# Kernel optimization log

Hardware: AMD Instinct MI355X
Metric: run time of the kernel (lower is better)

Reference implementation:

```python
import jax, jax.numpy as jnp
import numpy as np

D_MODEL = 1024
D_STATE = 8          # max(8, 16 // 2)
D_CONV = 4
D_INNER = int(1.5 * D_MODEL)   # expand = max(1.5, 2*0.75)
DT_RANK = (D_MODEL + 15) // 16 # 64
D_FF = 2 * D_MODEL
B, L = 2, 2048


def layer_norm(x, g, b, eps=1e-5):
    mu = jnp.mean(x, -1, keepdims=True)
    var = jnp.var(x, -1, keepdims=True)
    return (x - mu) * jax.lax.rsqrt(var + eps) * g + b


def setup_inputs() -> dict:
    key = jax.random.key(0)
    ks = jax.random.split(key, 12)
    def n(k, shape, scale=0.02):
        return jax.random.normal(k, shape, dtype=jnp.float32) * scale
    return {
        'x': jax.random.normal(ks[0], (B, L, D_MODEL), dtype=jnp.float32),
        'ln1_g': jnp.ones((D_MODEL,), jnp.float32),
        'ln1_b': jnp.zeros((D_MODEL,), jnp.float32),
        'ln2_g': jnp.ones((D_MODEL,), jnp.float32),
        'ln2_b': jnp.zeros((D_MODEL,), jnp.float32),
        'in_proj_w': n(ks[1], (2 * D_INNER, D_MODEL)),
        'conv_w': n(ks[2], (D_INNER, 1, D_CONV), 0.1),
        'conv_b': jnp.zeros((D_INNER,), jnp.float32),
        'x_proj_w': n(ks[3], (DT_RANK + 2 * D_STATE, D_INNER)),
        'dt_proj_w': n(ks[4], (D_INNER, DT_RANK), 0.1),
        'dt_proj_b': n(ks[5], (D_INNER,), 0.1),
        'A_log': jnp.log(jnp.broadcast_to(jnp.arange(1, D_STATE + 1, dtype=jnp.float32), (D_INNER, D_STATE))),
        'D': jnp.ones((D_INNER,), jnp.float32),
        'out_proj_w': n(ks[6], (D_MODEL, D_INNER)),
        'ffn_w1': n(ks[7], (D_FF, D_MODEL)),
        'ffn_b1': jnp.zeros((D_FF,), jnp.float32),
        'ffn_w2': n(ks[8], (D_MODEL, D_FF)),
        'ffn_b2': jnp.zeros((D_MODEL,), jnp.float32),
    }


def mamba(x, in_proj_w, conv_w, conv_b, x_proj_w, dt_proj_w, dt_proj_b, A_log, Dp, out_proj_w):
    # in_proj -> (x, z)
    xz = x @ in_proj_w.T                       # (B, L, 2*d_inner)
    xi, z = jnp.split(xz, 2, axis=-1)
    # depthwise causal conv over seq, kernel 4
    xc = jnp.transpose(xi, (0, 2, 1))          # (B, d_inner, L)
    xc = jax.lax.conv_general_dilated(
        xc, conv_w, window_strides=(1,), padding=[(D_CONV - 1, 0)],
        dimension_numbers=('NCH', 'OIH', 'NCH'), feature_group_count=D_INNER)
    xc = xc + conv_b[None, :, None]
    u = jax.nn.silu(jnp.transpose(xc, (0, 2, 1)))  # (B, L, d_inner)
    # x_proj -> dt, B, C
    x_dbl = u @ x_proj_w.T
    dt = x_dbl[..., :DT_RANK]
    Bm = x_dbl[..., DT_RANK:DT_RANK + D_STATE]
    Cm = x_dbl[..., DT_RANK + D_STATE:]
    delta = jax.nn.softplus(dt @ dt_proj_w.T + dt_proj_b)  # (B, L, d_inner)
    A = -jnp.exp(A_log)                                    # (d_inner, d_state)
    dA = jnp.exp(jnp.einsum('bld,dn->bldn', delta, A))     # (B, L, d_inner, d_state)
    dBu = jnp.einsum('bld,bln,bld->bldn', delta, Bm, u)
    # selective scan over time
    def step(h, inputs):
        dA_t, dBu_t, C_t = inputs
        h = dA_t * h + dBu_t                   # (B, d_inner, d_state)
        y = jnp.einsum('bdn,bn->bd', h, C_t)
        return h, y
    h0 = jnp.zeros((x.shape[0], D_INNER, D_STATE), x.dtype)
    _, ys = jax.lax.scan(step, h0, (jnp.moveaxis(dA, 1, 0), jnp.moveaxis(dBu, 1, 0), jnp.moveaxis(Cm, 1, 0)))
    y = jnp.moveaxis(ys, 0, 1) + u * Dp        # skip connection D*u
    y = y * jax.nn.silu(z)                     # gate
    return y @ out_proj_w.T


def reference(x, ln1_g, ln1_b, ln2_g, ln2_b, in_proj_w, conv_w, conv_b, x_proj_w,
              dt_proj_w, dt_proj_b, A_log, D, out_proj_w, ffn_w1, ffn_b1, ffn_w2, ffn_b2):
    residual = x
    xp = layer_norm(x, ln1_g, ln1_b)
    x = mamba(xp, in_proj_w, conv_w, conv_b, x_proj_w, dt_proj_w, dt_proj_b, A_log, D, out_proj_w) + residual
    xn = layer_norm(x, ln2_g, ln2_b)
    h = jax.nn.gelu(xn @ ffn_w1.T + ffn_b1, approximate=False)  # dropout is identity in eval
    return x + (h @ ffn_w2.T + ffn_b2)
```

## Files before the change

### kernel.cpp

```cpp
#include <hip/hip_runtime.h>
#include <math.h>

#define D_MODEL 1024
#define D_STATE 8
#define D_CONV  4
#define D_INNER 1536
#define DT_RANK 64
#define D_FF    2048
#define BATCH   2
#define SEQ     2048
#define NROWS   (BATCH*SEQ)
#define NC      32
#define LC      (SEQ/NC)
#define XPAD    128

typedef short bf16x8 __attribute__((ext_vector_type(8)));
typedef unsigned short u16x8 __attribute__((ext_vector_type(8)));
typedef float f32x4  __attribute__((ext_vector_type(4)));

__device__ inline unsigned short f2bf(float x) {
    union { float f; unsigned u; } v; v.f = x;
    unsigned r = v.u + 0x7fffu + ((v.u >> 16) & 1u);
    return (unsigned short)(r >> 16);
}
__device__ inline float bf2f(unsigned short h) {
    union { unsigned u; float f; } v; v.u = ((unsigned)h) << 16;
    return v.f;
}
__device__ inline float softplus_f(float x) {
    return (x > 20.0f) ? x : log1pf(__expf(x));
}
__device__ inline float gelu_f(float x) {
    return 0.5f * x * (1.0f + erff(x * 0.70710678118654752f));
}
__device__ inline float silu_f(float x) {
    return x / (1.0f + __expf(-x));
}
__device__ inline void gload16(const unsigned short* g, unsigned short* l) {
    typedef unsigned int u32;
    __builtin_amdgcn_global_load_lds(
        (const __attribute__((address_space(1))) u32*)g,
        (__attribute__((address_space(3))) u32*)l, 16, 0, 0);
}

#define PHASE_SYNC_PRE()  do { __builtin_amdgcn_s_barrier(); __builtin_amdgcn_sched_barrier(0); \
                               asm volatile("s_waitcnt lgkmcnt(0)" ::: "memory"); \
                               __builtin_amdgcn_sched_barrier(0); } while (0)
#define PHASE_SYNC_POST() do { __builtin_amdgcn_s_barrier(); __builtin_amdgcn_sched_barrier(0); } while (0)

__global__ __launch_bounds__(256) void wconv(const float* __restrict__ s0, unsigned short* __restrict__ d0,
                                             const float* __restrict__ s1, unsigned short* __restrict__ d1,
                                             const float* __restrict__ s2, unsigned short* __restrict__ d2,
                                             const float* __restrict__ s3, unsigned short* __restrict__ d3,
                                             const float* __restrict__ s4, unsigned short* __restrict__ d4) {
    int b = blockIdx.x;
    const float* s; unsigned short* d; int base;
    if      (b < 1536) { s = s0; d = d0; base = b * 2048; }
    else if (b < 1584) { s = s1; d = d1; base = (b - 1536) * 2048; }
    else if (b < 2352) { s = s2; d = d2; base = (b - 1584) * 2048; }
    else if (b < 3376) { s = s3; d = d3; base = (b - 2352) * 2048; }
    else               { s = s4; d = d4; base = (b - 3376) * 2048; }
    int i = base + threadIdx.x * 8;
    float4 v0 = *(const float4*)(s + i);
    float4 v1 = *(const float4*)(s + i + 4);
    ushort4 a, c;
    a.x = f2bf(v0.x); a.y = f2bf(v0.y); a.z = f2bf(v0.z); a.w = f2bf(v0.w);
    c.x = f2bf(v1.x); c.y = f2bf(v1.y); c.z = f2bf(v1.z); c.w = f2bf(v1.w);
    *(ushort4*)(d + i)     = a;
    *(ushort4*)(d + i + 4) = c;
}

__global__ __launch_bounds__(256) void xproj_pad(const float* __restrict__ src, unsigned short* __restrict__ dst) {
    int row = blockIdx.x;
    for (int c = threadIdx.x; c < D_INNER; c += 256)
        dst[row * D_INNER + c] = (row < 80) ? f2bf(src[row * D_INNER + c]) : (unsigned short)0;
}

__global__ __launch_bounds__(256) void ln_kernel(const float* __restrict__ x,
                                                 const float* __restrict__ g,
                                                 const float* __restrict__ b,
                                                 unsigned short* __restrict__ out) {
    __shared__ float sbuf[4];
    int row = blockIdx.x;
    int t = threadIdx.x;
    const float4* xr = (const float4*)(x + (size_t)row * D_MODEL);
    float4 v = xr[t];
    float s = v.x + v.y + v.z + v.w;
    for (int o = 32; o; o >>= 1) s += __shfl_down(s, o, 64);
    if ((t & 63) == 0) sbuf[t >> 6] = s;
    __syncthreads();
    float mu = (sbuf[0] + sbuf[1] + sbuf[2] + sbuf[3]) * (1.0f / D_MODEL);
    __syncthreads();
    float d0 = v.x - mu, d1 = v.y - mu, d2 = v.z - mu, d3 = v.w - mu;
    float q = d0*d0 + d1*d1 + d2*d2 + d3*d3;
    for (int o = 32; o; o >>= 1) q += __shfl_down(q, o, 64);
    if ((t & 63) == 0) sbuf[t >> 6] = q;
    __syncthreads();
    float var = (sbuf[0] + sbuf[1] + sbuf[2] + sbuf[3]) * (1.0f / D_MODEL);
    float rs = rsqrtf(var + 1e-5f);
    float4 gv = ((const float4*)g)[t];
    float4 bv = ((const float4*)b)[t];
    ushort4 st;
    st.x = f2bf(d0 * rs * gv.x + bv.x);
    st.y = f2bf(d1 * rs * gv.y + bv.y);
    st.z = f2bf(d2 * rs * gv.z + bv.z);
    st.w = f2bf(d3 * rs * gv.w + bv.w);
    ((ushort4*)(out + (size_t)row * D_MODEL))[t] = st;
}

#define EPI_F32        0
#define EPI_F32_BF16   1
#define EPI_SOFTPLUS   2
#define EPI_RESID      3
#define EPI_GELU_BF16  4
#define EPI_BIAS_RESID 5
#define EPI_BF16       6

template<int WN, int EPI, int SPLITK>
__global__ __launch_bounds__(512, 2) void gemm8p(
    const unsigned short* __restrict__ A, int lda,
    const unsigned short* __restrict__ Bm, int ldb, int K,
    float* __restrict__ Cf, unsigned short* __restrict__ Cb, int ldc,
    const float* __restrict__ bias,
    const float* __restrict__ resid, int ldr) {
    constexpr int WM = 8 / WN;
    constexpr int BN = WN * 64;
    constexpr int RW = 256 / WM;
    constexpr int CW = 64;
    constexpr int MI = RW / 16;
    constexpr int NI = CW / 16;
    constexpr int MIH = MI / 2, NIH = NI / 2;
    constexpr int ABYTES = 256 * 128;
    constexpr int BBYTES = BN * 128;
    constexpr int BOFF = 2 * ABYTES;
    __shared__ unsigned short lds[(2 * ABYTES + 2 * BBYTES) / 2];

    const int t = threadIdx.x, l = t & 63, w = t >> 6;
    const int wr = w / WN, wc = w % WN;

    const int nx = gridDim.x;
    const int nwg = nx * gridDim.y;
    int bid = blockIdx.y * nx + blockIdx.x;
    int q = nwg >> 3;
    int swz = (bid & 7) * q + (bid >> 3);
    const int m0 = (swz / nx) * 256, n0 = (swz % nx) * BN;
    const int kbase = (SPLITK > 1) ? blockIdx.z * K : 0;

    const int sr = l >> 3;
    const int sj = ((l & 7) * 16) ^ ((l >> 3) << 4);
    const int row_l = w * 8;
    const int row_c = (w >> 2) * 64 + (w & 3) * 8;

    auto STG = [&](int bufbyte, int rowbase, const unsigned short* G, int ldg, int gbase, int kt) {
        unsigned short* dst = (unsigned short*)((char*)lds + bufbyte + rowbase * 128);
        const unsigned short* src = G + (size_t)(gbase + rowbase + sr) * ldg + kbase + kt * 64 + (sj >> 1);
        gload16(src, dst);
    };
    auto S_Ah0 = [&](int b, int kt) {
        if (WN == 4) { STG(b * ABYTES, row_l, A, lda, m0, kt);       STG(b * ABYTES, 128 + row_l, A, lda, m0, kt); }
        else         { STG(b * ABYTES, row_c, A, lda, m0, kt);       STG(b * ABYTES, 128 + row_c, A, lda, m0, kt); }
    };
    auto S_Ah1 = [&](int b, int kt) {
        if (WN == 4) { STG(b * ABYTES, 64 + row_l, A, lda, m0, kt);  STG(b * ABYTES, 192 + row_l, A, lda, m0, kt); }
        else         { STG(b * ABYTES, 32 + row_c, A, lda, m0, kt);  STG(b * ABYTES, 160 + row_c, A, lda, m0, kt); }
    };
    auto S_Bc0 = [&](int b, int kt) {
        if (WN == 4) { STG(BOFF + b * BBYTES, row_c, Bm, ldb, n0, kt); STG(BOFF + b * BBYTES, 128 + row_c, Bm, ldb, n0, kt); }
        else         { STG(BOFF + b * BBYTES, row_c, Bm, ldb, n0, kt); }
    };
    auto S_Bc1 = [&](int b, int kt) {
        if (WN == 4) { STG(BOFF + b * BBYTES, 32 + row_c, Bm, ldb, n0, kt); STG(BOFF + b * BBYTES, 160 + row_c, Bm, ldb, n0, kt); }
        else         { STG(BOFF + b * BBYTES, 32 + row_c, Bm, ldb, n0, kt); }
    };

    auto LD = [&](int bytebase, int row, int kb) -> bf16x8 {
        int o = bytebase + row * 128 + (kb ^ ((row & 7) << 4));
        return *(const bf16x8*)((const char*)lds + o);
    };

    f32x4 acc[MI][NI] = {};
    bf16x8 af[MIH][2], b0v[NIH][2], b1v[NIH][2];

    auto LDA_set = [&](int buf, int qr, auto& dst) {
        #pragma unroll
        for (int mi = 0; mi < MIH; mi++)
            #pragma unroll
            for (int ks = 0; ks < 2; ks++)
                dst[mi][ks] = LD(buf * ABYTES, wr * RW + qr * (RW / 2) + mi * 16 + (l & 15),
                                 ks * 64 + (l >> 4) * 16);
    };
    auto LDB_set = [&](int buf, int qc, auto& dst) {
        #pragma unroll
        for (int ni2 = 0; ni2 < NIH; ni2++)
            #pragma unroll
            for (int ks = 0; ks < 2; ks++)
                dst[ni2][ks] = LD(BOFF + buf * BBYTES, wc * CW + qc * 32 + ni2 * 16 + (l & 15),
                                  ks * 64 + (l >> 4) * 16);
    };
    auto MFMA_Q = [&](int qr, int qc, auto& a_, auto& b_) {
        __builtin_amdgcn_s_setprio(1);
        #pragma unroll
        for (int mi = 0; mi < MIH; mi++)
            #pragma unroll
            for (int ni2 = 0; ni2 < NIH; ni2++)
                #pragma unroll
                for (int ks = 0; ks < 2; ks++)
                    acc[qr * MIH + mi][qc * NIH + ni2] =
                        __builtin_amdgcn_mfma_f32_16x16x32_bf16(a_[mi][ks], b_[ni2][ks],
                                                                acc[qr * MIH + mi][qc * NIH + ni2], 0, 0, 0);
        __builtin_amdgcn_s_setprio(0);
    };
    auto VMW = [&](bool last) {
        if (last)            asm volatile("s_waitcnt vmcnt(0)" ::: "memory");
        else if (WN == 4)    asm volatile("s_waitcnt vmcnt(6)" ::: "memory");
        else                 asm volatile("s_waitcnt vmcnt(5)" ::: "memory");
        __builtin_amdgcn_sched_barrier(0);
    };

    const int ni_ = K >> 7;

    S_Ah0(0, 0); S_Ah1(0, 0); S_Bc0(0, 0); S_Bc1(0, 0);
    S_Ah0(1, 1); S_Ah1(1, 1); S_Bc0(1, 1); S_Bc1(1, 1);
    if (WN == 4) asm volatile("s_waitcnt vmcnt(8)" ::: "memory");
    else         asm volatile("s_waitcnt vmcnt(6)" ::: "memory");
    __builtin_amdgcn_s_barrier();
    __builtin_amdgcn_sched_barrier(0);

    for (int i = 0; i < ni_; i++) {
        const bool last = (i == ni_ - 1);
        const int t2 = 2 * i + 2, t3 = 2 * i + 3;
        LDA_set(0, 0, af); LDB_set(0, 0, b0v);
        if (i) S_Bc0(1, 2 * i + 1);
        PHASE_SYNC_PRE(); MFMA_Q(0, 0, af, b0v); PHASE_SYNC_POST();
        LDB_set(0, 1, b1v);
        if (!last) S_Ah0(0, t2);
        PHASE_SYNC_PRE(); MFMA_Q(0, 1, af, b1v); PHASE_SYNC_POST();
        LDA_set(0, 1, af);
        PHASE_SYNC_PRE(); MFMA_Q(1, 1, af, b1v); PHASE_SYNC_POST();
        LDB_set(0, 0, b0v);
        if (!last) { S_Ah1(0, t2); S_Bc1(0, t2); }
        VMW(last);
        PHASE_SYNC_PRE(); MFMA_Q(1, 0, af, b0v); PHASE_SYNC_POST();
        LDA_set(1, 0, af); LDB_set(1, 0, b0v);
        if (!last) S_Bc0(0, t2);
        PHASE_SYNC_PRE(); MFMA_Q(0, 0, af, b0v); PHASE_SYNC_POST();
        LDB_set(1, 1, b1v);
        if (!last) S_Ah0(1, t3);
        PHASE_SYNC_PRE(); MFMA_Q(0, 1, af, b1v); PHASE_SYNC_POST();
        LDA_set(1, 1, af);
        PHASE_SYNC_PRE(); MFMA_Q(1, 1, af, b1v); PHASE_SYNC_POST();
        LDB_set(1, 0, b0v);
        if (!last) { S_Ah1(1, t3); S_Bc1(1, t3); }
        VMW(last);
        PHASE_SYNC_PRE(); MFMA_Q(1, 0, af, b0v); PHASE_SYNC_POST();
    }

    float* Cfp = Cf;
    if (SPLITK > 1) Cfp += (size_t)blockIdx.z * NROWS * ldc;
    #pragma unroll
    for (int ni2 = 0; ni2 < NI; ni2++) {
        int col = n0 + wc * CW + ni2 * 16 + (l & 15);
        float bv = 0.0f;
        if (EPI == EPI_SOFTPLUS || EPI == EPI_GELU_BF16 || EPI == EPI_BIAS_RESID) bv = bias[col];
        #pragma unroll
        for (int mi = 0; mi < MI; mi++) {
            #pragma unroll
            for (int j = 0; j < 4; j++) {
                int row = m0 + wr * RW + mi * 16 + (l >> 4) * 4 + j;
                float v = acc[mi][ni2][j];
                if (EPI == EPI_SOFTPLUS)        v = softplus_f(v + bv);
                else if (EPI == EPI_GELU_BF16)  v = gelu_f(v + bv);
                else if (EPI == EPI_RESID)      v = v + resid[(size_t)row * ldr + col];
                else if (EPI == EPI_BIAS_RESID) v = v + bv + resid[(size_t)row * ldr + col];
                if (EPI == EPI_GELU_BF16 || EPI == EPI_BF16) {
                    Cb[(size_t)row * ldc + col] = f2bf(v);
                } else {
                    Cfp[(size_t)row * ldc + col] = v;
                    if (EPI == EPI_F32_BF16) Cb[(size_t)row * ldc + col] = f2bf(v);
                }
            }
        }
    }
}

template<int WITH_BIAS>
__global__ __launch_bounds__(256) void sk2_reduce(const float* __restrict__ p,
                                                  const float* __restrict__ bias,
                                                  const float* __restrict__ resid,
                                                  float* __restrict__ o) {
    int i = (blockIdx.x * 256 + threadIdx.x) * 4;
    const size_t seg = (size_t)NROWS * D_MODEL;
    float4 a = *(const float4*)(p + i);
    float4 b = *(const float4*)(p + i + seg);
    float4 r = *(const float4*)(resid + i);
    float4 o4;
    if (WITH_BIAS) {
        float4 bb = *(const float4*)(bias + (i & (D_MODEL - 1)));
        o4.x = a.x + b.x + r.x + bb.x;
        o4.y = a.y + b.y + r.y + bb.y;
        o4.z = a.z + b.z + r.z + bb.z;
        o4.w = a.w + b.w + r.w + bb.w;
    } else {
        o4.x = a.x + b.x + r.x;
        o4.y = a.y + b.y + r.y;
        o4.z = a.z + b.z + r.z;
        o4.w = a.w + b.w + r.w;
    }
    *(float4*)(o + i) = o4;
}

template<int EPI, int SPLITK>
__global__ __launch_bounds__(256) void gemm_mfma(
    const unsigned short* __restrict__ A, int lda,
    const unsigned short* __restrict__ B, int ldb, int K,
    float* __restrict__ Cf, unsigned short* __restrict__ Cb, int ldc,
    const float* __restrict__ bias,
    const float* __restrict__ resid, int ldr) {
    __shared__ unsigned short As[3][128 * 32];
    __shared__ unsigned short Bs[3][128 * 32];
    int t = threadIdx.x, l = t & 63, w = t >> 6;
    int nx = gridDim.x;
    int nwg = nx * gridDim.y;
    int bid = blockIdx.y * nx + blockIdx.x;
    int q = nwg >> 3;
    int swz = (bid & 7) * q + (bid >> 3);
    int m0 = (swz / nx) * 128, n0 = (swz % nx) * 128;
    int kbase = (SPLITK > 1) ? blockIdx.z * K : 0;
    int c0 = 2 * w, c1 = 2 * w + 1;
    int srow = l >> 2, scol = (l & 3) * 8;
    const unsigned short* Ag0 = A + (size_t)(m0 + 16 * c0 + srow) * lda + kbase + scol;
    const unsigned short* Ag1 = A + (size_t)(m0 + 16 * c1 + srow) * lda + kbase + scol;
    const unsigned short* Bg0 = B + (size_t)(n0 + 16 * c0 + srow) * ldb + kbase + scol;
    const unsigned short* Bg1 = B + (size_t)(n0 + 16 * c1 + srow) * ldb + kbase + scol;
    int wr = w >> 1, wc = w & 1;
    int aoff = (wr * 64 + (l & 15)) * 32 + (l >> 4) * 8;
    int boff = (wc * 64 + (l & 15)) * 32 + (l >> 4) * 8;

    f32x4 acc[4][4] = {};
    int nt = K >> 5;

    gload16(Ag0, &As[0][c0 * 512]);
    gload16(Ag1, &As[0][c1 * 512]);
    gload16(Bg0, &Bs[0][c0 * 512]);
    gload16(Bg1, &Bs[0][c1 * 512]);
    if (nt > 1) {
        gload16(Ag0 + 32, &As[1][c0 * 512]);
        gload16(Ag1 + 32, &As[1][c1 * 512]);
        gload16(Bg0 + 32, &Bs[1][c0 * 512]);
        gload16(Bg1 + 32, &Bs[1][c1 * 512]);
    }

    int cur = 0;
    for (int ti = 0; ti < nt; ti++) {
        int pf = ti + 2;
        if (pf < nt) {
            int nb = cur - 1; if (nb < 0) nb += 3;
            int k0 = pf << 5;
            gload16(Ag0 + k0, &As[nb][c0 * 512]);
            gload16(Ag1 + k0, &As[nb][c1 * 512]);
            gload16(Bg0 + k0, &Bs[nb][c0 * 512]);
            gload16(Bg1 + k0, &Bs[nb][c1 * 512]);
        }
        int rem = nt - 1 - ti;
        if (rem >= 2)      asm volatile("s_waitcnt vmcnt(8)" ::: "memory");
        else if (rem == 1) asm volatile("s_waitcnt vmcnt(4)" ::: "memory");
        else               asm volatile("s_waitcnt vmcnt(0)" ::: "memory");
        __builtin_amdgcn_s_barrier();

        const unsigned short* Ab = &As[cur][0];
        const unsigned short* Bb = &Bs[cur][0];
        bf16x8 af[4], bfv[4];
        #pragma unroll
        for (int i = 0; i < 4; i++) af[i] = *(const bf16x8*)(Ab + aoff + i * 512);
        #pragma unroll
        for (int i = 0; i < 4; i++) bfv[i] = *(const bf16x8*)(Bb + boff + i * 512);
        __builtin_amdgcn_s_setprio(1);
        #pragma unroll
        for (int mi = 0; mi < 4; mi++)
            #pragma unroll
            for (int ni = 0; ni < 4; ni++)
                acc[mi][ni] = __builtin_amdgcn_mfma_f32_16x16x32_bf16(af[mi], bfv[ni], acc[mi][ni], 0, 0, 0);
        __builtin_amdgcn_s_setprio(0);
        __builtin_amdgcn_s_barrier();
        cur++; if (cur == 3) cur = 0;
    }

    if (SPLITK > 1) Cf += (size_t)blockIdx.z * NROWS * ldc;
    int colb = n0 + wc * 64 + (l & 15);
    int rowb = m0 + wr * 64 + (l >> 4) * 4;
    #pragma unroll
    for (int ni = 0; ni < 4; ni++) {
        int col = colb + ni * 16;
        float bv = 0.0f;
        if (EPI == EPI_SOFTPLUS || EPI == EPI_GELU_BF16 || EPI == EPI_BIAS_RESID) bv = bias[col];
        #pragma unroll
        for (int mi = 0; mi < 4; mi++) {
            #pragma unroll
            for (int j = 0; j < 4; j++) {
                int row = rowb + mi * 16 + j;
                float v = acc[mi][ni][j];
                if (EPI == EPI_SOFTPLUS)        v = softplus_f(v + bv);
                else if (EPI == EPI_GELU_BF16)  v = gelu_f(v + bv);
                else if (EPI == EPI_RESID)      v = v + resid[(size_t)row * ldr + col];
                else if (EPI == EPI_BIAS_RESID) v = v + bv + resid[(size_t)row * ldr + col];
                if (EPI == EPI_GELU_BF16 || EPI == EPI_BF16) {
                    Cb[(size_t)row * ldc + col] = f2bf(v);
                } else {
                    Cf[(size_t)row * ldc + col] = v;
                    if (EPI == EPI_F32_BF16) Cb[(size_t)row * ldc + col] = f2bf(v);
                }
            }
        }
    }
}

__global__ __launch_bounds__(256) void xdbl_reduce(const float* __restrict__ part,
                                                   float* __restrict__ xdbl,
                                                   unsigned short* __restrict__ xdbl_bf) {
    int i = blockIdx.x * 256 + threadIdx.x;
    const size_t seg = (size_t)NROWS * XPAD;
    float s = part[i] + part[i + seg] + part[i + 2 * seg] + part[i + 3 * seg];
    xdbl[i] = s;
    xdbl_bf[i] = f2bf(s);
}

__global__ __launch_bounds__(256) void conv_silu(const unsigned short* __restrict__ xz,
                                                 const float* __restrict__ w,
                                                 const float* __restrict__ cb,
                                                 unsigned short* __restrict__ u) {
    int idx = (blockIdx.x * 256 + threadIdx.x) * 8;
    int d = idx % D_INNER;
    int bl = idx / D_INNER;
    int l = bl & (SEQ - 1);
    float acc[8];
    float4 wv[8];
    #pragma unroll
    for (int j = 0; j < 8; j++) wv[j] = *(const float4*)(w + (d + j) * 4);
    float4 cb0 = *(const float4*)(cb + d);
    float4 cb1 = *(const float4*)(cb + d + 4);
    acc[0] = cb0.x; acc[1] = cb0.y; acc[2] = cb0.z; acc[3] = cb0.w;
    acc[4] = cb1.x; acc[5] = cb1.y; acc[6] = cb1.z; acc[7] = cb1.w;
    #pragma unroll
    for (int k = 0; k < 4; k++) {
        int lp = l - 3 + k;
        if (lp >= 0) {
            u16x8 s = *(const u16x8*)(xz + (size_t)(bl - 3 + k) * (2 * D_INNER) + d);
            #pragma unroll
            for (int j = 0; j < 8; j++) {
                float wk = (k == 0) ? wv[j].x : (k == 1) ? wv[j].y : (k == 2) ? wv[j].z : wv[j].w;
                acc[j] += bf2f((unsigned short)s[j]) * wk;
            }
        }
    }
    u16x8 o;
    #pragma unroll
    for (int j = 0; j < 8; j++) o[j] = f2bf(silu_f(acc[j]));
    *(u16x8*)(u + idx) = o;
}

__global__ __launch_bounds__(256) void scan_passA(const float* __restrict__ delta,
                                                  const unsigned short* __restrict__ u,
                                                  const float* __restrict__ xdbl,
                                                  const float* __restrict__ A_log,
                                                  float* __restrict__ P,
                                                  float* __restrict__ S) {
    int d = blockIdx.x * 256 + threadIdx.x;
    int c = blockIdx.y, b = blockIdx.z;
    __shared__ float bc[LC][16];
    int base_row = b * SEQ + c * LC;
    for (int e = threadIdx.x; e < LC * 16; e += 256) {
        int lrr = e >> 4, col = e & 15;
        bc[lrr][col] = xdbl[(size_t)(base_row + lrr) * XPAD + DT_RANK + col];
    }
    __syncthreads();
    float Ad[8];
    #pragma unroll
    for (int n = 0; n < 8; n++) Ad[n] = -__expf(A_log[d * 8 + n]);
    float prod[8], hs[8];
    #pragma unroll
    for (int n = 0; n < 8; n++) { prod[n] = 1.0f; hs[n] = 0.0f; }
    for (int lrr = 0; lrr < LC; lrr++) {
        int row = base_row + lrr;
        float dl = delta[(size_t)row * D_INNER + d];
        float uu = bf2f(u[(size_t)row * D_INNER + d]);
        float du = dl * uu;
        #pragma unroll
        for (int n = 0; n < 8; n++) {
            float dA = __expf(dl * Ad[n]);
            prod[n] *= dA;
            hs[n] = dA * hs[n] + du * bc[lrr][n];
        }
    }
    size_t o = ((size_t)((size_t)b * NC + c) * D_INNER + d) * 8;
    #pragma unroll
    for (int n = 0; n < 8; n++) { P[o + n] = prod[n]; S[o + n] = hs[n]; }
}

__global__ __launch_bounds__(256) void scan_passB(const float* __restrict__ P,
                                                  const float* __restrict__ S,
                                                  float* __restrict__ hstart) {
    int tid = blockIdx.x * 256 + threadIdx.x;
    int b = tid / (D_INNER * 8);
    int rem = tid % (D_INNER * 8);
    float h = 0.0f;
    for (int c = 0; c < NC; c++) {
        size_t o = (size_t)(b * NC + c) * (D_INNER * 8) + rem;
        hstart[o] = h;
        h = P[o] * h + S[o];
    }
}

__global__ __launch_bounds__(256) void scan_passC(const float* __restrict__ delta,
                                                  const unsigned short* __restrict__ u,
                                                  const float* __restrict__ xdbl,
                                                  const float* __restrict__ A_log,
                                                  const float* __restrict__ hstart,
                                                  const unsigned short* __restrict__ xz,
                                                  const float* __restrict__ Dp,
                                                  unsigned short* __restrict__ ygate) {
    int d = blockIdx.x * 256 + threadIdx.x;
    int c = blockIdx.y, b = blockIdx.z;
    __shared__ float bc[LC][16];
    int base_row = b * SEQ + c * LC;
    for (int e = threadIdx.x; e < LC * 16; e += 256) {
        int lrr = e >> 4, col = e & 15;
        bc[lrr][col] = xdbl[(size_t)(base_row + lrr) * XPAD + DT_RANK + col];
    }
    __syncthreads();
    float Ad[8];
    #pragma unroll
    for (int n = 0; n < 8; n++) Ad[n] = -__expf(A_log[d * 8 + n]);
    float h[8];
    size_t ho = ((size_t)((size_t)b * NC + c) * D_INNER + d) * 8;
    #pragma unroll
    for (int n = 0; n < 8; n++) h[n] = hstart[ho + n];
    float Dd = Dp[d];
    for (int lrr = 0; lrr < LC; lrr++) {
        int row = base_row + lrr;
        float dl = delta[(size_t)row * D_INNER + d];
        float uu = bf2f(u[(size_t)row * D_INNER + d]);
        float du = dl * uu;
        float y = 0.0f;
        #pragma unroll
        for (int n = 0; n < 8; n++) {
            float dA = __expf(dl * Ad[n]);
            h[n] = dA * h[n] + du * bc[lrr][n];
            y += h[n] * bc[lrr][8 + n];
        }
        y += uu * Dd;
        float z = bf2f(xz[(size_t)row * (2 * D_INNER) + D_INNER + d]);
        ygate[(size_t)row * D_INNER + d] = f2bf(y * silu_f(z));
    }
}

extern "C" void kernel_launch(void* const* d_in, const int* in_sizes, int n_in,
                              void* d_out, int out_size, void* d_ws, size_t ws_size,
                              hipStream_t stream) {
    const float* x         = (const float*)d_in[0];
    const float* ln1_g     = (const float*)d_in[1];
    const float* ln1_b     = (const float*)d_in[2];
    const float* ln2_g     = (const float*)d_in[3];
    const float* ln2_b     = (const float*)d_in[4];
    const float* in_proj_w = (const float*)d_in[5];
    const float* conv_w    = (const float*)d_in[6];
    const float* conv_b    = (const float*)d_in[7];
    const float* x_proj_w  = (const float*)d_in[8];
    const float* dt_proj_w = (const float*)d_in[9];
    const float* dt_proj_b = (const float*)d_in[10];
    const float* A_log     = (const float*)d_in[11];
    const float* Dp        = (const float*)d_in[12];
    const float* out_proj_w= (const float*)d_in[13];
    const float* ffn_w1    = (const float*)d_in[14];
    const float* ffn_b1    = (const float*)d_in[15];
    const float* ffn_w2    = (const float*)d_in[16];
    const float* ffn_b2    = (const float*)d_in[17];
    float* out = (float*)d_out;

    float* xdbl  = (float*)d_ws;
    float* delta = xdbl + (size_t)NROWS * XPAD;
    float* P     = delta + (size_t)NROWS * D_INNER;
    float* S     = P + (size_t)BATCH * NC * D_INNER * 8;
    float* hst   = S + (size_t)BATCH * NC * D_INNER * 8;
    float* x2    = hst + (size_t)BATCH * NC * D_INNER * 8;
    float* part  = x2;
    float* psum  = delta;
    unsigned short* xz_bf   = (unsigned short*)(x2 + (size_t)NROWS * D_MODEL);
    unsigned short* xp_bf   = xz_bf + (size_t)NROWS * 2 * D_INNER;
    unsigned short* u_bf    = xp_bf + (size_t)NROWS * D_MODEL;
    unsigned short* xdbl_bf = u_bf + (size_t)NROWS * D_INNER;
    unsigned short* yg_bf   = xdbl_bf + (size_t)NROWS * XPAD;
    unsigned short* w_in    = yg_bf + (size_t)NROWS * D_INNER;
    unsigned short* w_xp    = w_in + (size_t)2 * D_INNER * D_MODEL;
    unsigned short* w_dt    = w_xp + (size_t)XPAD * D_INNER;
    unsigned short* w_out   = w_dt + (size_t)D_INNER * DT_RANK;
    unsigned short* w_f1    = w_out + (size_t)D_MODEL * D_INNER;
    unsigned short* w_f2    = w_f1 + (size_t)D_FF * D_MODEL;
    unsigned short* hff_bf  = xz_bf;

    wconv<<<4400, 256, 0, stream>>>(in_proj_w, w_in, dt_proj_w, w_dt, out_proj_w, w_out,
                                    ffn_w1, w_f1, ffn_w2, w_f2);
    xproj_pad<<<XPAD, 256, 0, stream>>>(x_proj_w, w_xp);
    ln_kernel<<<NROWS, 256, 0, stream>>>(x, ln1_g, ln1_b, xp_bf);
    gemm8p<4, EPI_BF16, 1><<<dim3(3072 / 256, NROWS / 256), 512, 0, stream>>>(
        xp_bf, D_MODEL, w_in, D_MODEL, D_MODEL, nullptr, xz_bf, 2 * D_INNER, nullptr, nullptr, 0);
    conv_silu<<<(NROWS * D_INNER) / (256 * 8), 256, 0, stream>>>(xz_bf, conv_w, conv_b, u_bf);
    gemm_mfma<EPI_F32, 4><<<dim3(1, NROWS / 128, 4), 256, 0, stream>>>(
        u_bf, D_INNER, w_xp, D_INNER, D_INNER / 4, part, nullptr, XPAD, nullptr, nullptr, 0);
    xdbl_reduce<<<(NROWS * XPAD) / 256, 256, 0, stream>>>(part, xdbl, xdbl_bf);
    gemm_mfma<EPI_SOFTPLUS, 1><<<dim3(D_INNER / 128, NROWS / 128), 256, 0, stream>>>(
        xdbl_bf, XPAD, w_dt, DT_RANK, DT_RANK, delta, nullptr, D_INNER, dt_proj_b, nullptr, 0);
    scan_passA<<<dim3(D_INNER / 256, NC, BATCH), 256, 0, stream>>>(delta, u_bf, xdbl, A_log, P, S);
    scan_passB<<<(BATCH * D_INNER * 8) / 256, 256, 0, stream>>>(P, S, hst);
    scan_passC<<<dim3(D_INNER / 256, NC, BATCH), 256, 0, stream>>>(delta, u_bf, xdbl, A_log, hst, xz_bf, Dp, yg_bf);
    gemm8p<2, EPI_F32, 2><<<dim3(D_MODEL / 128, NROWS / 256, 2), 512, 0, stream>>>(
        yg_bf, D_INNER, w_out, D_INNER, D_INNER / 2, psum, nullptr, D_MODEL, nullptr, nullptr, 0);
    sk2_reduce<0><<<(NROWS * D_MODEL) / 1024, 256, 0, stream>>>(psum, nullptr, x, x2);
    ln_kernel<<<NROWS, 256, 0, stream>>>(x2, ln2_g, ln2_b, xp_bf);
    gemm8p<2, EPI_GELU_BF16, 1><<<dim3(D_FF / 128, NROWS / 256), 512, 0, stream>>>(
        xp_bf, D_MODEL, w_f1, D_MODEL, D_MODEL, nullptr, hff_bf, D_FF, ffn_b1, nullptr, 0);
    gemm8p<2, EPI_F32, 2><<<dim3(D_MODEL / 128, NROWS / 256, 2), 512, 0, stream>>>(
        hff_bf, D_FF, w_f2, D_FF, D_FF / 2, psum, nullptr, D_MODEL, nullptr, nullptr, 0);
    sk2_reduce<1><<<(NROWS * D_MODEL) / 1024, 256, 0, stream>>>(psum, ffn_b2, x2, out);
}
```

Before: 290.4 us.

## Fuse prep kernels, fuse split-K reduce with LayerNorm, store delta as bf16

Merges the weight conversion, x_proj padding and first LayerNorm into one prep kernel, and fuses the out_proj split-K reduction with the second LayerNorm. Stores the softplus delta output in bf16 instead of fp32, which halves the scan passes' delta traffic at some cost in precision. Removes the sched_barrier calls around the gemm8p phase syncs and the vmcnt waits, which gives the compiler more freedom to schedule but may break the hand-tuned ordering. Also reorganizes the workspace so psum no longer aliases delta.

Result: faster. 281.1 us (-3.2%).

```diff
diff --git a/kernel.cpp b/kernel.cpp
--- a/kernel.cpp
+++ b/kernel.cpp
@@ -43,37 +43,66 @@
         (__attribute__((address_space(3))) u32*)l, 16, 0, 0);
 }
 
-#define PHASE_SYNC_PRE()  do { __builtin_amdgcn_s_barrier(); __builtin_amdgcn_sched_barrier(0); \
-                               asm volatile("s_waitcnt lgkmcnt(0)" ::: "memory"); \
-                               __builtin_amdgcn_sched_barrier(0); } while (0)
-#define PHASE_SYNC_POST() do { __builtin_amdgcn_s_barrier(); __builtin_amdgcn_sched_barrier(0); } while (0)
-
-__global__ __launch_bounds__(256) void wconv(const float* __restrict__ s0, unsigned short* __restrict__ d0,
-                                             const float* __restrict__ s1, unsigned short* __restrict__ d1,
-                                             const float* __restrict__ s2, unsigned short* __restrict__ d2,
-                                             const float* __restrict__ s3, unsigned short* __restrict__ d3,
-                                             const float* __restrict__ s4, unsigned short* __restrict__ d4) {
+#define PHASE_SYNC_PRE()  do { __builtin_amdgcn_s_barrier(); \
+                               asm volatile("s_waitcnt lgkmcnt(0)" ::: "memory"); } while (0)
+#define PHASE_SYNC_POST() do { __builtin_amdgcn_s_barrier(); } while (0)
+
+__global__ __launch_bounds__(256) void prep_kernel(
+    const float* __restrict__ s0, unsigned short* __restrict__ d0,
+    const float* __restrict__ s1, unsigned short* __restrict__ d1,
+    const float* __restrict__ s2, unsigned short* __restrict__ d2,
+    const float* __restrict__ s3, unsigned short* __restrict__ d3,
+    const float* __restrict__ s4, unsigned short* __restrict__ d4,
+    const float* __restrict__ xpw, unsigned short* __restrict__ xpd,
+    const float* __restrict__ x, const float* __restrict__ g1,
+    const float* __restrict__ b1, unsigned short* __restrict__ xout) {
     int b = blockIdx.x;
-    const float* s; unsigned short* d; int base;
-    if      (b < 1536) { s = s0; d = d0; base = b * 2048; }
-    else if (b < 1584) { s = s1; d = d1; base = (b - 1536) * 2048; }
-    else if (b < 2352) { s = s2; d = d2; base = (b - 1584) * 2048; }
-    else if (b < 3376) { s = s3; d = d3; base = (b - 2352) * 2048; }
-    else               { s = s4; d = d4; base = (b - 3376) * 2048; }
-    int i = base + threadIdx.x * 8;
-    float4 v0 = *(const float4*)(s + i);
-    float4 v1 = *(const float4*)(s + i + 4);
-    ushort4 a, c;
-    a.x = f2bf(v0.x); a.y = f2bf(v0.y); a.z = f2bf(v0.z); a.w = f2bf(v0.w);
-    c.x = f2bf(v1.x); c.y = f2bf(v1.y); c.z = f2bf(v1.z); c.w = f2bf(v1.w);
-    *(ushort4*)(d + i)     = a;
-    *(ushort4*)(d + i + 4) = c;
-}
-
-__global__ __launch_bounds__(256) void xproj_pad(const float* __restrict__ src, unsigned short* __restrict__ dst) {
-    int row = blockIdx.x;
-    for (int c = threadIdx.x; c < D_INNER; c += 256)
-        dst[row * D_INNER + c] = (row < 80) ? f2bf(src[row * D_INNER + c]) : (unsigned short)0;
+    if (b < 4400) {
+        const float* s; unsigned short* d; int base;
+        if      (b < 1536) { s = s0; d = d0; base = b * 2048; }
+        else if (b < 1584) { s = s1; d = d1; base = (b - 1536) * 2048; }
+        else if (b < 2352) { s = s2; d = d2; base = (b - 1584) * 2048; }
+        else if (b < 3376) { s = s3; d = d3; base = (b - 2352) * 2048; }
+        else               { s = s4; d = d4; base = (b - 3376) * 2048; }
+        int i = base + threadIdx.x * 8;
+        float4 v0 = *(const float4*)(s + i);
+        float4 v1 = *(const float4*)(s + i + 4);
+        ushort4 a, c;
+        a.x = f2bf(v0.x); a.y = f2bf(v0.y); a.z = f2bf(v0.z); a.w = f2bf(v0.w);
+        c.x = f2bf(v1.x); c.y = f2bf(v1.y); c.z = f2bf(v1.z); c.w = f2bf(v1.w);
+        *(ushort4*)(d + i)     = a;
+        *(ushort4*)(d + i + 4) = c;
+    } else if (b < 4528) {
+        int row = b - 4400;
+        for (int c = threadIdx.x; c < D_INNER; c += 256)
+            xpd[row * D_INNER + c] = (row < 80) ? f2bf(xpw[row * D_INNER + c]) : (unsigned short)0;
+    } else {
+        __shared__ float sbuf[4];
+        int row = b - 4528;
+        int t = threadIdx.x;
+        float4 v = ((const float4*)(x + (size_t)row * D_MODEL))[t];
+        float s = v.x + v.y + v.z + v.w;
+        for (int o = 32; o; o >>= 1) s += __shfl_down(s, o, 64);
+        if ((t & 63) == 0) sbuf[t >> 6] = s;
+        __syncthreads();
+        float mu = (sbuf[0] + sbuf[1] + sbuf[2] + sbuf[3]) * (1.0f / D_MODEL);
+        __syncthreads();
+        float e0 = v.x - mu, e1 = v.y - mu, e2 = v.z - mu, e3 = v.w - mu;
+        float q = e0*e0 + e1*e1 + e2*e2 + e3*e3;
+        for (int o = 32; o; o >>= 1) q += __shfl_down(q, o, 64);
+        if ((t & 63) == 0) sbuf[t >> 6] = q;
+        __syncthreads();
+        float var = (sbuf[0] + sbuf[1] + sbuf[2] + sbuf[3]) * (1.0f / D_MODEL);
+        float rs = rsqrtf(var + 1e-5f);
+        float4 gv = ((const float4*)g1)[t];
+        float4 bv = ((const float4*)b1)[t];
+        ushort4 st;
+        st.x = f2bf(e0 * rs * gv.x + bv.x);
+        st.y = f2bf(e1 * rs * gv.y + bv.y);
+        st.z = f2bf(e2 * rs * gv.z + bv.z);
+        st.w = f2bf(e3 * rs * gv.w + bv.w);
+        ((ushort4*)(xout + (size_t)row * D_MODEL))[t] = st;
+    }
 }
 
 __global__ __launch_bounds__(256) void ln_kernel(const float* __restrict__ x,
@@ -83,8 +112,7 @@
     __shared__ float sbuf[4];
     int row = blockIdx.x;
     int t = threadIdx.x;
-    const float4* xr = (const float4*)(x + (size_t)row * D_MODEL);
-    float4 v = xr[t];
+    float4 v = ((const float4*)(x + (size_t)row * D_MODEL))[t];
     float s = v.x + v.y + v.z + v.w;
     for (int o = 32; o; o >>= 1) s += __shfl_down(s, o, 64);
     if ((t & 63) == 0) sbuf[t >> 6] = s;
@@ -115,6 +143,7 @@
 #define EPI_GELU_BF16  4
 #define EPI_BIAS_RESID 5
 #define EPI_BF16       6
+#define EPI_SOFTPLUS_BF16 7
 
 template<int WN, int EPI, int SPLITK>
 __global__ __launch_bounds__(512, 2) void gemm8p(
@@ -214,7 +243,6 @@
         if (last)            asm volatile("s_waitcnt vmcnt(0)" ::: "memory");
         else if (WN == 4)    asm volatile("s_waitcnt vmcnt(6)" ::: "memory");
         else                 asm volatile("s_waitcnt vmcnt(5)" ::: "memory");
-        __builtin_amdgcn_sched_barrier(0);
     };
 
     const int ni_ = K >> 7;
@@ -224,7 +252,6 @@
     if (WN == 4) asm volatile("s_waitcnt vmcnt(8)" ::: "memory");
     else         asm volatile("s_waitcnt vmcnt(6)" ::: "memory");
     __builtin_amdgcn_s_barrier();
-    __builtin_amdgcn_sched_barrier(0);
 
     for (int i = 0; i < ni_; i++) {
         const bool last = (i == ni_ - 1);
@@ -283,7 +310,49 @@
     }
 }
 
-template<int WITH_BIAS>
+__global__ __launch_bounds__(256) void sk2_ln(const float* __restrict__ p,
+                                              const float* __restrict__ resid,
+                                              const float* __restrict__ g,
+                                              const float* __restrict__ b,
+                                              float* __restrict__ x2,
+                                              unsigned short* __restrict__ xn) {
+    __shared__ float sbuf[4];
+    int row = blockIdx.x;
+    int t = threadIdx.x;
+    const size_t seg = (size_t)NROWS * D_MODEL;
+    size_t base = (size_t)row * D_MODEL + t * 4;
+    float4 a = *(const float4*)(p + base);
+    float4 bb = *(const float4*)(p + base + seg);
+    float4 r = *(const float4*)(resid + base);
+    float4 v;
+    v.x = a.x + bb.x + r.x;
+    v.y = a.y + bb.y + r.y;
+    v.z = a.z + bb.z + r.z;
+    v.w = a.w + bb.w + r.w;
+    *(float4*)(x2 + base) = v;
+    float s = v.x + v.y + v.z + v.w;
+    for (int o = 32; o; o >>= 1) s += __shfl_down(s, o, 64);
+    if ((t & 63) == 0) sbuf[t >> 6] = s;
+    __syncthreads();
+    float mu = (sbuf[0] + sbuf[1] + sbuf[2] + sbuf[3]) * (1.0f / D_MODEL);
+    __syncthreads();
+    float d0 = v.x - mu, d1 = v.y - mu, d2 = v.z - mu, d3 = v.w - mu;
+    float qq = d0*d0 + d1*d1 + d2*d2 + d3*d3;
+    for (int o = 32; o; o >>= 1) qq += __shfl_down(qq, o, 64);
+    if ((t & 63) == 0) sbuf[t >> 6] = qq;
+    __syncthreads();
+    float var = (sbuf[0] + sbuf[1] + sbuf[2] + sbuf[3]) * (1.0f / D_MODEL);
+    float rs = rsqrtf(var + 1e-5f);
+    float4 gv = ((const float4*)g)[t];
+    float4 bv = ((const float4*)b)[t];
+    ushort4 st;
+    st.x = f2bf(d0 * rs * gv.x + bv.x);
+    st.y = f2bf(d1 * rs * gv.y + bv.y);
+    st.z = f2bf(d2 * rs * gv.z + bv.z);
+    st.w = f2bf(d3 * rs * gv.w + bv.w);
+    ((ushort4*)(xn + (size_t)row * D_MODEL))[t] = st;
+}
+
 __global__ __launch_bounds__(256) void sk2_reduce(const float* __restrict__ p,
                                                   const float* __restrict__ bias,
                                                   const float* __restrict__ resid,
@@ -293,19 +362,12 @@
     float4 a = *(const float4*)(p + i);
     float4 b = *(const float4*)(p + i + seg);
     float4 r = *(const float4*)(resid + i);
+    float4 bb = *(const float4*)(bias + (i & (D_MODEL - 1)));
     float4 o4;
-    if (WITH_BIAS) {
-        float4 bb = *(const float4*)(bias + (i & (D_MODEL - 1)));
-        o4.x = a.x + b.x + r.x + bb.x;
-        o4.y = a.y + b.y + r.y + bb.y;
-        o4.z = a.z + b.z + r.z + bb.z;
-        o4.w = a.w + b.w + r.w + bb.w;
-    } else {
-        o4.x = a.x + b.x + r.x;
-        o4.y = a.y + b.y + r.y;
-        o4.z = a.z + b.z + r.z;
-        o4.w = a.w + b.w + r.w;
-    }
+    o4.x = a.x + b.x + r.x + bb.x;
+    o4.y = a.y + b.y + r.y + bb.y;
+    o4.z = a.z + b.z + r.z + bb.z;
+    o4.w = a.w + b.w + r.w + bb.w;
     *(float4*)(o + i) = o4;
 }
 
@@ -392,18 +454,18 @@
     for (int ni = 0; ni < 4; ni++) {
         int col = colb + ni * 16;
         float bv = 0.0f;
-        if (EPI == EPI_SOFTPLUS || EPI == EPI_GELU_BF16 || EPI == EPI_BIAS_RESID) bv = bias[col];
+        if (EPI == EPI_SOFTPLUS || EPI == EPI_GELU_BF16 || EPI == EPI_BIAS_RESID || EPI == EPI_SOFTPLUS_BF16) bv = bias[col];
         #pragma unroll
         for (int mi = 0; mi < 4; mi++) {
             #pragma unroll
             for (int j = 0; j < 4; j++) {
                 int row = rowb + mi * 16 + j;
                 float v = acc[mi][ni][j];
-                if (EPI == EPI_SOFTPLUS)        v = softplus_f(v + bv);
+                if (EPI == EPI_SOFTPLUS || EPI == EPI_SOFTPLUS_BF16) v = softplus_f(v + bv);
                 else if (EPI == EPI_GELU_BF16)  v = gelu_f(v + bv);
                 else if (EPI == EPI_RESID)      v = v + resid[(size_t)row * ldr + col];
                 else if (EPI == EPI_BIAS_RESID) v = v + bv + resid[(size_t)row * ldr + col];
-                if (EPI == EPI_GELU_BF16 || EPI == EPI_BF16) {
+                if (EPI == EPI_GELU_BF16 || EPI == EPI_BF16 || EPI == EPI_SOFTPLUS_BF16) {
                     Cb[(size_t)row * ldc + col] = f2bf(v);
                 } else {
                     Cf[(size_t)row * ldc + col] = v;
@@ -458,7 +520,7 @@
     *(u16x8*)(u + idx) = o;
 }
 
-__global__ __launch_bounds__(256) void scan_passA(const float* __restrict__ delta,
+__global__ __launch_bounds__(256) void scan_passA(const unsigned short* __restrict__ delta,
                                                   const unsigned short* __restrict__ u,
                                                   const float* __restrict__ xdbl,
                                                   const float* __restrict__ A_log,
@@ -481,7 +543,7 @@
     for (int n = 0; n < 8; n++) { prod[n] = 1.0f; hs[n] = 0.0f; }
     for (int lrr = 0; lrr < LC; lrr++) {
         int row = base_row + lrr;
-        float dl = delta[(size_t)row * D_INNER + d];
+        float dl = bf2f(delta[(size_t)row * D_INNER + d]);
         float uu = bf2f(u[(size_t)row * D_INNER + d]);
         float du = dl * uu;
         #pragma unroll
@@ -510,7 +572,7 @@
     }
 }
 
-__global__ __launch_bounds__(256) void scan_passC(const float* __restrict__ delta,
+__global__ __launch_bounds__(256) void scan_passC(const unsigned short* __restrict__ delta,
                                                   const unsigned short* __restrict__ u,
                                                   const float* __restrict__ xdbl,
                                                   const float* __restrict__ A_log,
@@ -537,7 +599,7 @@
     float Dd = Dp[d];
     for (int lrr = 0; lrr < LC; lrr++) {
         int row = base_row + lrr;
-        float dl = delta[(size_t)row * D_INNER + d];
+        float dl = bf2f(delta[(size_t)row * D_INNER + d]);
         float uu = bf2f(u[(size_t)row * D_INNER + d]);
         float du = dl * uu;
         float y = 0.0f;
@@ -577,19 +639,19 @@
     float* out = (float*)d_out;
 
     float* xdbl  = (float*)d_ws;
-    float* delta = xdbl + (size_t)NROWS * XPAD;
-    float* P     = delta + (size_t)NROWS * D_INNER;
+    float* P     = xdbl + (size_t)NROWS * XPAD;
     float* S     = P + (size_t)BATCH * NC * D_INNER * 8;
     float* hst   = S + (size_t)BATCH * NC * D_INNER * 8;
     float* x2    = hst + (size_t)BATCH * NC * D_INNER * 8;
-    float* part  = x2;
-    float* psum  = delta;
-    unsigned short* xz_bf   = (unsigned short*)(x2 + (size_t)NROWS * D_MODEL);
+    float* psum  = x2 + (size_t)NROWS * D_MODEL;
+    float* part  = psum;
+    unsigned short* xz_bf   = (unsigned short*)(psum + 2 * (size_t)NROWS * D_MODEL);
     unsigned short* xp_bf   = xz_bf + (size_t)NROWS * 2 * D_INNER;
     unsigned short* u_bf    = xp_bf + (size_t)NROWS * D_MODEL;
     unsigned short* xdbl_bf = u_bf + (size_t)NROWS * D_INNER;
     unsigned short* yg_bf   = xdbl_bf + (size_t)NROWS * XPAD;
-    unsigned short* w_in    = yg_bf + (size_t)NROWS * D_INNER;
+    unsigned short* dl_bf   = yg_bf + (size_t)NROWS * D_INNER;
+    unsigned short* w_in    = dl_bf + (size_t)NROWS * D_INNER;
     unsigned short* w_xp    = w_in + (size_t)2 * D_INNER * D_MODEL;
     unsigned short* w_dt    = w_xp + (size_t)XPAD * D_INNER;
     unsigned short* w_out   = w_dt + (size_t)D_INNER * DT_RANK;
@@ -597,28 +659,26 @@
     unsigned short* w_f2    = w_f1 + (size_t)D_FF * D_MODEL;
     unsigned short* hff_bf  = xz_bf;
 
-    wconv<<<4400, 256, 0, stream>>>(in_proj_w, w_in, dt_proj_w, w_dt, out_proj_w, w_out,
-                                    ffn_w1, w_f1, ffn_w2, w_f2);
-    xproj_pad<<<XPAD, 256, 0, stream>>>(x_proj_w, w_xp);
-    ln_kernel<<<NROWS, 256, 0, stream>>>(x, ln1_g, ln1_b, xp_bf);
+    prep_kernel<<<4400 + XPAD + NROWS, 256, 0, stream>>>(
+        in_proj_w, w_in, dt_proj_w, w_dt, out_proj_w, w_out, ffn_w1, w_f1, ffn_w2, w_f2,
+        x_proj_w, w_xp, x, ln1_g, ln1_b, xp_bf);
     gemm8p<4, EPI_BF16, 1><<<dim3(3072 / 256, NROWS / 256), 512, 0, stream>>>(
         xp_bf, D_MODEL, w_in, D_MODEL, D_MODEL, nullptr, xz_bf, 2 * D_INNER, nullptr, nullptr, 0);
     conv_silu<<<(NROWS * D_INNER) / (256 * 8), 256, 0, stream>>>(xz_bf, conv_w, conv_b, u_bf);
     gemm_mfma<EPI_F32, 4><<<dim3(1, NROWS / 128, 4), 256, 0, stream>>>(
         u_bf, D_INNER, w_xp, D_INNER, D_INNER / 4, part, nullptr, XPAD, nullptr, nullptr, 0);
     xdbl_reduce<<<(NROWS * XPAD) / 256, 256, 0, stream>>>(part, xdbl, xdbl_bf);
-    gemm_mfma<EPI_SOFTPLUS, 1><<<dim3(D_INNER / 128, NROWS / 128), 256, 0, stream>>>(
-        xdbl_bf, XPAD, w_dt, DT_RANK, DT_RANK, delta, nullptr, D_INNER, dt_proj_b, nullptr, 0);
-    scan_passA<<<dim3(D_INNER / 256, NC, BATCH), 256, 0, stream>>>(delta, u_bf, xdbl, A_log, P, S);
+    gemm_mfma<EPI_SOFTPLUS_BF16, 1><<<dim3(D_INNER / 128, NROWS / 128), 256, 0, stream>>>(
+        xdbl_bf, XPAD, w_dt, DT_RANK, DT_RANK, nullptr, dl_bf, D_INNER, dt_proj_b, nullptr, 0);
+    scan_passA<<<dim3(D_INNER / 256, NC, BATCH), 256, 0, stream>>>(dl_bf, u_bf, xdbl, A_log, P, S);
     scan_passB<<<(BATCH * D_INNER * 8) / 256, 256, 0, stream>>>(P, S, hst);
-    scan_passC<<<dim3(D_INNER / 256, NC, BATCH), 256, 0, stream>>>(delta, u_bf, xdbl, A_log, hst, xz_bf, Dp, yg_bf);
+    scan_passC<<<dim3(D_INNER / 256, NC, BATCH), 256, 0, stream>>>(dl_bf, u_bf, xdbl, A_log, hst, xz_bf, Dp, yg_bf);
     gemm8p<2, EPI_F32, 2><<<dim3(D_MODEL / 128, NROWS / 256, 2), 512, 0, stream>>>(
         yg_bf, D_INNER, w_out, D_INNER, D_INNER / 2, psum, nullptr, D_MODEL, nullptr, nullptr, 0);
-    sk2_reduce<0><<<(NROWS * D_MODEL) / 1024, 256, 0, stream>>>(psum, nullptr, x, x2);
-    ln_kernel<<<NROWS, 256, 0, stream>>>(x2, ln2_g, ln2_b, xp_bf);
+    sk2_ln<<<NROWS, 256, 0, stream>>>(psum, x, ln2_g, ln2_b, x2, xp_bf);
     gemm8p<2, EPI_GELU_BF16, 1><<<dim3(D_FF / 128, NROWS / 256), 512, 0, stream>>>(
         xp_bf, D_MODEL, w_f1, D_MODEL, D_MODEL, nullptr, hff_bf, D_FF, ffn_b1, nullptr, 0);
     gemm8p<2, EPI_F32, 2><<<dim3(D_MODEL / 128, NROWS / 256, 2), 512, 0, stream>>>(
         hff_bf, D_FF, w_f2, D_FF, D_FF / 2, psum, nullptr, D_MODEL, nullptr, nullptr, 0);
-    sk2_reduce<1><<<(NROWS * D_MODEL) / 1024, 256, 0, stream>>>(psum, ffn_b2, x2, out);
-}
+    sk2_reduce<<<(NROWS * D_MODEL) / 1024, 256, 0, stream>>>(psum, ffn_b2, x2, out);
+}
```
